# Kernel optimization log

Hardware: AMD Instinct MI355X
Metric: run time of the kernel (lower is better)

## Reference

```python
import jax, jax.numpy as jnp
import numpy as np

HEADS = 8
DIM_HEAD = 80
BATCH_SIZE = 2  # cfg batch (module init kwarg)


def setup_inputs() -> dict:
    key = jax.random.key(0)
    ks = jax.random.split(key, 6)
    F, S, D = 16, 1024, 640  # frames*batch, latent HW, query_dim
    hidden_states = jax.random.normal(ks[0], (F, S, D), jnp.float32)
    Wq = jax.random.normal(ks[1], (D, D), jnp.float32) * 0.02
    Wk = jax.random.normal(ks[2], (D, D), jnp.float32) * 0.02
    Wv = jax.random.normal(ks[3], (D, D), jnp.float32) * 0.02
    Wo = jax.random.normal(ks[4], (D, D), jnp.float32) * 0.02
    bo = jax.random.normal(ks[5], (D,), jnp.float32) * 0.02
    return {"hidden_states": hidden_states, "Wq": Wq, "Wk": Wk, "Wv": Wv, "Wo": Wo, "bo": bo}


def reference(hidden_states, Wq, Wk, Wv, Wo, bo):
    F, S, D = hidden_states.shape
    h, d = HEADS, DIM_HEAD
    scale = d ** -0.5

    q = hidden_states @ Wq  # [F, S, D]
    k = hidden_states @ Wk
    v = hidden_states @ Wv

    # cross-frame trick: replace every frame's K/V with the FIRST frame of its batch group
    vl = 1 if F < BATCH_SIZE else F // BATCH_SIZE  # video_length
    g = F // vl  # batch groups
    k = jnp.broadcast_to(k.reshape(g, vl, S, D)[:, :1], (g, vl, S, D)).reshape(F, S, D)
    v = jnp.broadcast_to(v.reshape(g, vl, S, D)[:, :1], (g, vl, S, D)).reshape(F, S, D)

    def to_heads(t):  # [F, S, h*d] -> [F*h, S, d]
        return t.reshape(F, S, h, d).transpose(0, 2, 1, 3).reshape(F * h, S, d)

    qh, kh, vh = to_heads(q), to_heads(k), to_heads(v)

    scores = jnp.einsum('bid,bjd->bij', qh, kh) * scale  # [F*h, S, S]
    probs = jax.nn.softmax(scores, axis=-1)
    out = jnp.einsum('bij,bjd->bid', probs, vh)  # [F*h, S, d]

    out = out.reshape(F, h, S, d).transpose(0, 2, 1, 3).reshape(F, S, h * d)
    return out @ Wo + bo
```

## Files before the change

kernel.cpp:

```cpp
#include <hip/hip_runtime.h>
#include <hip/hip_bf16.h>

typedef unsigned short u16;
typedef unsigned int u32;
typedef __attribute__((ext_vector_type(8))) short bf16x8;
typedef __attribute__((ext_vector_type(4))) float f32x4;

#define D640 640

__device__ __forceinline__ float b2f(u16 u) {
  union { u32 i; float f; } x; x.i = ((u32)u) << 16; return x.f;
}
__device__ __forceinline__ u16 f2b(float f) {
  union { __hip_bfloat16 h; u16 u; } c; c.h = __float2bfloat16(f); return c.u;
}
__device__ __forceinline__ u32 pack2(float a, float b) {
  union { __hip_bfloat162 h; u32 u; } c;
  c.h.x = __float2bfloat16(a); c.h.y = __float2bfloat16(b); return c.u;
}
__device__ __forceinline__ bf16x8 pack8(f32x4 lo, f32x4 hi) {
  bf16x8 r;
  r[0] = (short)f2b(lo[0]); r[1] = (short)f2b(lo[1]);
  r[2] = (short)f2b(lo[2]); r[3] = (short)f2b(lo[3]);
  r[4] = (short)f2b(hi[0]); r[5] = (short)f2b(hi[1]);
  r[6] = (short)f2b(hi[2]); r[7] = (short)f2b(hi[3]);
  return r;
}

__global__ void detect_dtype(const u16* __restrict__ hs, u32* __restrict__ flag) {
  __shared__ u32 cnt;
  if (threadIdx.x == 0) cnt = 0;
  __syncthreads();
  int plaus = 0;
#pragma unroll
  for (int i = 0; i < 16; ++i) {
    u16 u = hs[(threadIdx.x * 16 + i) * 2];
    u32 e = (u >> 7) & 0xFF;
    if ((e >= 0x70 && e <= 0x8F) || (u & 0x7FFF) == 0) plaus++;
  }
  atomicAdd(&cnt, (u32)plaus);
  __syncthreads();
  if (threadIdx.x == 0) *flag = (cnt < 2048) ? 1u : 0u;
}

__global__ __launch_bounds__(256) void transpose_w(
    const void* __restrict__ w0, const void* __restrict__ w1,
    const void* __restrict__ w2, const void* __restrict__ w3,
    u16* __restrict__ out, const u32* __restrict__ flag)
{
  __shared__ u16 t[32][33];
  const bool isF32 = (*flag != 0);
  const void* src = blockIdx.z == 0 ? w0 : blockIdx.z == 1 ? w1 : blockIdx.z == 2 ? w2 : w3;
  u16* dst = out + (size_t)blockIdx.z * 409600;
  int tx = threadIdx.x, ty = threadIdx.y;
  int x = blockIdx.x * 32 + tx;
  int y = blockIdx.y * 32 + ty;
  if (isF32) {
    const float* s = (const float*)src;
#pragma unroll
    for (int j = 0; j < 32; j += 8) t[ty + j][tx] = f2b(s[(y + j) * D640 + x]);
  } else {
    const u16* s = (const u16*)src;
#pragma unroll
    for (int j = 0; j < 32; j += 8) t[ty + j][tx] = s[(y + j) * D640 + x];
  }
  __syncthreads();
  int x2 = blockIdx.y * 32 + tx;
  int y2 = blockIdx.x * 32 + ty;
#pragma unroll
  for (int j = 0; j < 32; j += 8) dst[(y2 + j) * D640 + x2] = t[tx][ty + j];
}

__device__ __forceinline__ void gemm_body(
    const void* __restrict__ Av, const u16* __restrict__ BT, void* __restrict__ Cv,
    float scale, bool isF32, int aRow0, int cMode, int bx, int by)
{
  __shared__ __align__(16) u16 Asub[128 * 32];
  __shared__ __align__(16) u16 Bsub[128 * 32];
  const bool aF32 = isF32;
  const int tid = threadIdx.x;
  const int lane = tid & 63, w = tid >> 6;
  const int wr = w >> 1, wc = w & 1;
  const int l15 = lane & 15, g = lane >> 4;
  const int rowBase = bx * 128;
  const int colBase = by * 128;

  const int r0 = tid >> 2, r1 = r0 + 64, gc = tid & 3;
  const int ls0 = r0 * 4 + (gc ^ ((r0 >> 1) & 3));
  const int ls1 = r1 * 4 + (gc ^ ((r1 >> 1) & 3));
  const size_t aIdx0 = (size_t)(aRow0 + rowBase + r0) * D640 + gc * 8;
  const size_t aIdx1 = (size_t)(aRow0 + rowBase + r1) * D640 + gc * 8;
  const u16* Bg0 = BT + (colBase + r0) * D640 + gc * 8;
  const u16* Bg1 = BT + (colBase + r1) * D640 + gc * 8;

  int aoff[4], boff[4];
#pragma unroll
  for (int f = 0; f < 4; ++f) {
    int R = wr * 64 + f * 16 + l15;
    aoff[f] = (R * 4 + (g ^ ((R >> 1) & 3))) * 8;
    int Cc = wc * 64 + f * 16 + l15;
    boff[f] = (Cc * 4 + (g ^ ((Cc >> 1) & 3))) * 8;
  }

  f32x4 acc[4][4];
#pragma unroll
  for (int i = 0; i < 4; ++i)
#pragma unroll
    for (int j = 0; j < 4; ++j) acc[i][j] = (f32x4){0.f, 0.f, 0.f, 0.f};

  bf16x8 ra0, ra1, rb0, rb1;
  if (aF32) {
    const float* Af = (const float*)Av;
    ra0 = pack8(*(const f32x4*)(Af + aIdx0), *(const f32x4*)(Af + aIdx0 + 4));
    ra1 = pack8(*(const f32x4*)(Af + aIdx1), *(const f32x4*)(Af + aIdx1 + 4));
  } else {
    const u16* Ab = (const u16*)Av;
    ra0 = *(const bf16x8*)(Ab + aIdx0);
    ra1 = *(const bf16x8*)(Ab + aIdx1);
  }
  rb0 = *(const bf16x8*)Bg0;
  rb1 = *(const bf16x8*)Bg1;

  for (int kt = 0; kt < 20; ++kt) {
    __syncthreads();
    *(bf16x8*)&Asub[ls0 * 8] = ra0;
    *(bf16x8*)&Asub[ls1 * 8] = ra1;
    *(bf16x8*)&Bsub[ls0 * 8] = rb0;
    *(bf16x8*)&Bsub[ls1 * 8] = rb1;
    __syncthreads();
    if (kt < 19) {
      const int k1 = (kt + 1) * 32;
      if (aF32) {
        const float* Af = (const float*)Av;
        ra0 = pack8(*(const f32x4*)(Af + aIdx0 + k1), *(const f32x4*)(Af + aIdx0 + k1 + 4));
        ra1 = pack8(*(const f32x4*)(Af + aIdx1 + k1), *(const f32x4*)(Af + aIdx1 + k1 + 4));
      } else {
        const u16* Ab = (const u16*)Av;
        ra0 = *(const bf16x8*)(Ab + aIdx0 + k1);
        ra1 = *(const bf16x8*)(Ab + aIdx1 + k1);
      }
      rb0 = *(const bf16x8*)(Bg0 + k1);
      rb1 = *(const bf16x8*)(Bg1 + k1);
    }
    bf16x8 a[4], b[4];
#pragma unroll
    for (int f = 0; f < 4; ++f) a[f] = *(const bf16x8*)&Asub[aoff[f]];
#pragma unroll
    for (int f = 0; f < 4; ++f) b[f] = *(const bf16x8*)&Bsub[boff[f]];
    __builtin_amdgcn_s_setprio(1);
#pragma unroll
    for (int i = 0; i < 4; ++i)
#pragma unroll
      for (int j = 0; j < 4; ++j)
        acc[i][j] = __builtin_amdgcn_mfma_f32_16x16x32_bf16(a[i], b[j], acc[i][j], 0, 0, 0);
    __builtin_amdgcn_s_setprio(0);
  }

#pragma unroll
  for (int j = 0; j < 4; ++j) {
    int col = colBase + wc * 64 + j * 16 + l15;
#pragma unroll
    for (int i = 0; i < 4; ++i) {
      int row = rowBase + wr * 64 + i * 16 + g * 4;
#pragma unroll
      for (int r = 0; r < 4; ++r) {
        float v = acc[i][j][r] * scale;
        if (cMode == 2) {
          int rw = row + r;
          int rl = rw & 63;
          int slot = (rl & 32) | ((rl & 12) << 1) | (((rl >> 4) & 1) << 2) | (rl & 3);
          ((u16*)Cv)[(size_t)col * 1024 + (rw & ~63) + slot] = f2b(v);
        } else {
          ((u16*)Cv)[(size_t)(row + r) * D640 + col] = f2b(v);
        }
      }
    }
  }
}

__global__ __launch_bounds__(256) void gemm_kv(
    const void* __restrict__ hs, const u16* __restrict__ WTk, const u16* __restrict__ WTv,
    u16* __restrict__ Kb, u16* __restrict__ Vb, const u32* __restrict__ flag)
{
  const int z = blockIdx.z;
  const bool isK = (z < 2);
  const int grp = z & 1;
  const u16* bt = isK ? WTk : WTv;
  void* cv = isK ? (void*)(Kb + (size_t)grp * 1024 * 640)
                 : (void*)(Vb + (size_t)grp * 655360);
  gemm_body(hs, bt, cv, 1.f, (*flag != 0), grp * 8192, isK ? 0 : 2,
            blockIdx.x, blockIdx.y);
}

__global__ __launch_bounds__(256) void gemm2(
    const void* __restrict__ Av, const u16* __restrict__ BT, void* __restrict__ Cv,
    float scale, const void* __restrict__ bias, const u32* __restrict__ flag,
    int aF32mode, int cF32mode)
{
  __shared__ __align__(16) u16 Asub[128 * 32];
  __shared__ __align__(16) u16 Bsub[160 * 32];
  const bool isF32 = (*flag != 0);
  const bool aF32 = aF32mode && isF32;
  const bool cF32 = cF32mode && isF32;
  const int tid = threadIdx.x;
  const int lane = tid & 63, w = tid >> 6;
  const int wr = w >> 1, wc = w & 1;
  const int l15 = lane & 15, g = lane >> 4;
  const int rowBase = blockIdx.x * 128;
  const int colBase = blockIdx.y * 160;

  const int ar0 = tid >> 2, ar1 = ar0 + 64, gc = tid & 3;
  const int als0 = ar0 * 4 + (gc ^ ((ar0 >> 1) & 3));
  const int als1 = ar1 * 4 + (gc ^ ((ar1 >> 1) & 3));
  const size_t aIdx0 = (size_t)(rowBase + ar0) * D640 + gc * 8;
  const size_t aIdx1 = (size_t)(rowBase + ar1) * D640 + gc * 8;
  const bool hasB3 = (tid < 128);
  const int br0 = ar0, br1 = ar1, br2 = hasB3 ? (128 + (tid >> 2)) : 0;
  const int bls0 = als0, bls1 = als1;
  const int bls2 = br2 * 4 + (gc ^ ((br2 >> 1) & 3));
  const u16* Bg0 = BT + (colBase + br0) * D640 + gc * 8;
  const u16* Bg1 = BT + (colBase + br1) * D640 + gc * 8;
  const u16* Bg2 = BT + (colBase + br2) * D640 + gc * 8;

  int aoff[4], boff[5];
#pragma unroll
  for (int f = 0; f < 4; ++f) {
    int R = wr * 64 + f * 16 + l15;
    aoff[f] = (R * 4 + (g ^ ((R >> 1) & 3))) * 8;
  }
#pragma unroll
  for (int j = 0; j < 5; ++j) {
    int Cc = wc * 80 + j * 16 + l15;
    boff[j] = (Cc * 4 + (g ^ ((Cc >> 1) & 3))) * 8;
  }

  f32x4 acc[4][5];
#pragma unroll
  for (int i = 0; i < 4; ++i)
#pragma unroll
    for (int j = 0; j < 5; ++j) acc[i][j] = (f32x4){0.f, 0.f, 0.f, 0.f};

  bf16x8 ra0, ra1, rb0, rb1, rb2;
  if (aF32) {
    const float* Af = (const float*)Av;
    ra0 = pack8(*(const f32x4*)(Af + aIdx0), *(const f32x4*)(Af + aIdx0 + 4));
    ra1 = pack8(*(const f32x4*)(Af + aIdx1), *(const f32x4*)(Af + aIdx1 + 4));
  } else {
    const u16* Ab = (const u16*)Av;
    ra0 = *(const bf16x8*)(Ab + aIdx0);
    ra1 = *(const bf16x8*)(Ab + aIdx1);
  }
  rb0 = *(const bf16x8*)Bg0;
  rb1 = *(const bf16x8*)Bg1;
  rb2 = hasB3 ? *(const bf16x8*)Bg2 : (bf16x8){0,0,0,0,0,0,0,0};

  for (int kt = 0; kt < 20; ++kt) {
    __syncthreads();
    *(bf16x8*)&Asub[als0 * 8] = ra0;
    *(bf16x8*)&Asub[als1 * 8] = ra1;
    *(bf16x8*)&Bsub[bls0 * 8] = rb0;
    *(bf16x8*)&Bsub[bls1 * 8] = rb1;
    if (hasB3) *(bf16x8*)&Bsub[bls2 * 8] = rb2;
    __syncthreads();
    if (kt < 19) {
      const int k1 = (kt + 1) * 32;
      if (aF32) {
        const float* Af = (const float*)Av;
        ra0 = pack8(*(const f32x4*)(Af + aIdx0 + k1), *(const f32x4*)(Af + aIdx0 + k1 + 4));
        ra1 = pack8(*(const f32x4*)(Af + aIdx1 + k1), *(const f32x4*)(Af + aIdx1 + k1 + 4));
      } else {
        const u16* Ab = (const u16*)Av;
        ra0 = *(const bf16x8*)(Ab + aIdx0 + k1);
        ra1 = *(const bf16x8*)(Ab + aIdx1 + k1);
      }
      rb0 = *(const bf16x8*)(Bg0 + k1);
      rb1 = *(const bf16x8*)(Bg1 + k1);
      if (hasB3) rb2 = *(const bf16x8*)(Bg2 + k1);
    }
    bf16x8 a[4], b[5];
#pragma unroll
    for (int f = 0; f < 4; ++f) a[f] = *(const bf16x8*)&Asub[aoff[f]];
#pragma unroll
    for (int j = 0; j < 5; ++j) b[j] = *(const bf16x8*)&Bsub[boff[j]];
    __builtin_amdgcn_s_setprio(1);
#pragma unroll
    for (int i = 0; i < 4; ++i)
#pragma unroll
      for (int j = 0; j < 5; ++j)
        acc[i][j] = __builtin_amdgcn_mfma_f32_16x16x32_bf16(a[i], b[j], acc[i][j], 0, 0, 0);
    __builtin_amdgcn_s_setprio(0);
  }

#pragma unroll
  for (int j = 0; j < 5; ++j) {
    int col = colBase + wc * 80 + j * 16 + l15;
    float bb = 0.f;
    if (bias) bb = cF32 ? ((const float*)bias)[col] : b2f(((const u16*)bias)[col]);
#pragma unroll
    for (int i = 0; i < 4; ++i) {
      int row = rowBase + wr * 64 + i * 16 + g * 4;
#pragma unroll
      for (int r = 0; r < 4; ++r) {
        float v = acc[i][j][r] * scale + bb;
        if (cF32) ((float*)Cv)[(size_t)(row + r) * D640 + col] = v;
        else      ((u16*)Cv)[(size_t)(row + r) * D640 + col] = f2b(v);
      }
    }
  }
}

__global__ __launch_bounds__(256, 3) void attn_kernel(
    const u16* __restrict__ Q, const u16* __restrict__ K2,
    const u16* __restrict__ VT, u16* __restrict__ AO)
{
  __shared__ __align__(16) u16 Klds[64 * 104];
  __shared__ __align__(16) u16 Vlds[80 * 72];

  const int tid = threadIdx.x, lane = tid & 63, w = tid >> 6;
  const int l15 = lane & 15, g = lane >> 4;
  const int qc = blockIdx.x, bh = blockIdx.y;
  const int f = bh >> 3, h = bh & 7;
  const int grp = f >> 3;

  const u16* Qp = Q + (size_t)(f * 1024 + qc * 128 + w * 32) * D640 + h * 80;
  const u16* Kp = K2 + (size_t)(grp * 1024) * D640 + h * 80;
  const u16* Vp = VT + (size_t)(grp * 8 + h) * 80 * 1024;

  if (tid < 128) {
    const bf16x8 z8 = {0, 0, 0, 0, 0, 0, 0, 0};
    *(bf16x8*)&Klds[(tid >> 1) * 104 + 80 + (tid & 1) * 8] = z8;
  }

  bf16x8 qreg[2][3];
#pragma unroll
  for (int qb = 0; qb < 2; ++qb)
#pragma unroll
    for (int dc = 0; dc < 3; ++dc) {
      int dd = dc * 32 + g * 8;
      if (dd < 80) qreg[qb][dc] = *(const bf16x8*)(Qp + (l15 + 16 * qb) * D640 + dd);
      else         qreg[qb][dc] = (bf16x8){0, 0, 0, 0, 0, 0, 0, 0};
    }

  f32x4 acc[2][5];
#pragma unroll
  for (int qb = 0; qb < 2; ++qb)
#pragma unroll
    for (int db = 0; db < 5; ++db) acc[qb][db] = (f32x4){0.f, 0.f, 0.f, 0.f};
  float mreg[2] = {-1e30f, -1e30f};
  float lrow[2] = {0.f, 0.f};

  const u16* gsrc[5];
  u16* ldst[5];
  int step[5];
#pragma unroll
  for (int i = 0; i < 5; ++i) {
    int c = tid + i * 256;
    if (c < 640) {
      int row = c / 10, cc = c - row * 10;
      gsrc[i] = Kp + row * D640 + cc * 8;
      ldst[i] = &Klds[row * 104 + cc * 8];
      step[i] = 64 * D640;
    } else {
      int c2 = c - 640, d = c2 >> 3, cc = c2 & 7;
      gsrc[i] = Vp + d * 1024 + cc * 8;
      ldst[i] = &Vlds[d * 72 + cc * 8];
      step[i] = 64;
    }
  }

  bf16x8 pre[5];
#pragma unroll
  for (int i = 0; i < 5; ++i) pre[i] = *(const bf16x8*)gsrc[i];

  for (int it = 0; it < 16; ++it) {
    __syncthreads();
#pragma unroll
    for (int i = 0; i < 5; ++i) *(bf16x8*)ldst[i] = pre[i];
    __syncthreads();
    if (it < 15) {
#pragma unroll
      for (int i = 0; i < 5; ++i) pre[i] = *(const bf16x8*)(gsrc[i] + (it + 1) * step[i]);
    }

    f32x4 st[4][2];
#pragma unroll
    for (int kb = 0; kb < 4; ++kb)
#pragma unroll
      for (int qb = 0; qb < 2; ++qb) st[kb][qb] = (f32x4){0.f, 0.f, 0.f, 0.f};
    __builtin_amdgcn_s_setprio(1);
#pragma unroll
    for (int dc = 0; dc < 3; ++dc)
#pragma unroll
      for (int kb = 0; kb < 4; ++kb) {
        bf16x8 ka = *(const bf16x8*)&Klds[(kb * 16 + l15) * 104 + dc * 32 + g * 8];
        st[kb][0] = __builtin_amdgcn_mfma_f32_16x16x32_bf16(ka, qreg[0][dc], st[kb][0], 0, 0, 0);
        st[kb][1] = __builtin_amdgcn_mfma_f32_16x16x32_bf16(ka, qreg[1][dc], st[kb][1], 0, 0, 0);
      }
    __builtin_amdgcn_s_setprio(0);

    float mt[2];
#pragma unroll
    for (int qb = 0; qb < 2; ++qb) {
      float m01 = fmaxf(fmaxf(st[0][qb][0], st[0][qb][1]), fmaxf(st[0][qb][2], st[0][qb][3]));
      float m23 = fmaxf(fmaxf(st[1][qb][0], st[1][qb][1]), fmaxf(st[1][qb][2], st[1][qb][3]));
      float m45 = fmaxf(fmaxf(st[2][qb][0], st[2][qb][1]), fmaxf(st[2][qb][2], st[2][qb][3]));
      float m67 = fmaxf(fmaxf(st[3][qb][0], st[3][qb][1]), fmaxf(st[3][qb][2], st[3][qb][3]));
      float m = fmaxf(fmaxf(m01, m23), fmaxf(m45, m67));
      m = fmaxf(m, __shfl_xor(m, 16, 64));
      m = fmaxf(m, __shfl_xor(m, 32, 64));
      mt[qb] = m;
    }

    if (__any((mt[0] > mreg[0] + 8.f) || (mt[1] > mreg[1] + 8.f))) {
#pragma unroll
      for (int qb = 0; qb < 2; ++qb) {
        float mn = fmaxf(mreg[qb], mt[qb]);
        float scl = exp2f(mreg[qb] - mn);
        mreg[qb] = mn;
        lrow[qb] *= scl;
        float s_[4];
#pragma unroll
        for (int r = 0; r < 4; ++r)
          s_[r] = __shfl(scl, (lane & 48) | (g * 4 + r), 64);
#pragma unroll
        for (int db = 0; db < 5; ++db)
#pragma unroll
          for (int r = 0; r < 4; ++r) acc[qb][db][r] *= s_[r];
      }
    }

    bf16x8 pa[2][2];
#pragma unroll
    for (int qb = 0; qb < 2; ++qb) {
      float sum = 0.f;
      u32 wlo[4], whi[4];
#pragma unroll
      for (int kb = 0; kb < 4; ++kb) {
        float p0 = exp2f(st[kb][qb][0] - mreg[qb]);
        float p1 = exp2f(st[kb][qb][1] - mreg[qb]);
        float p2 = exp2f(st[kb][qb][2] - mreg[qb]);
        float p3 = exp2f(st[kb][qb][3] - mreg[qb]);
        sum += (p0 + p1) + (p2 + p3);
        wlo[kb] = pack2(p0, p1);
        whi[kb] = pack2(p2, p3);
      }
      sum += __shfl_xor(sum, 16, 64);
      sum += __shfl_xor(sum, 32, 64);
      lrow[qb] += sum;
#pragma unroll
      for (int kc = 0; kc < 2; ++kc) {
        union { u32 u[4]; bf16x8 v; } cvt;
        cvt.u[0] = wlo[2 * kc];
        cvt.u[1] = whi[2 * kc];
        cvt.u[2] = wlo[2 * kc + 1];
        cvt.u[3] = whi[2 * kc + 1];
        pa[qb][kc] = cvt.v;
      }
    }

    __builtin_amdgcn_s_setprio(1);
#pragma unroll
    for (int kc = 0; kc < 2; ++kc) {
#pragma unroll
      for (int db = 0; db < 5; ++db) {
        bf16x8 bv = *(const bf16x8*)&Vlds[(db * 16 + l15) * 72 + kc * 32 + g * 8];
        acc[0][db] = __builtin_amdgcn_mfma_f32_16x16x32_bf16(pa[0][kc], bv, acc[0][db], 0, 0, 0);
        acc[1][db] = __builtin_amdgcn_mfma_f32_16x16x32_bf16(pa[1][kc], bv, acc[1][db], 0, 0, 0);
      }
    }
    __builtin_amdgcn_s_setprio(0);
  }

  u16* Op = AO + (size_t)(f * 1024 + qc * 128 + w * 32) * D640 + h * 80;
#pragma unroll
  for (int qb = 0; qb < 2; ++qb) {
    float i_[4];
#pragma unroll
    for (int r = 0; r < 4; ++r)
      i_[r] = 1.f / __shfl(lrow[qb], (lane & 48) | (g * 4 + r), 64);
#pragma unroll
    for (int db = 0; db < 5; ++db)
#pragma unroll
      for (int r = 0; r < 4; ++r)
        Op[(qb * 16 + g * 4 + r) * D640 + db * 16 + l15] = f2b(acc[qb][db][r] * i_[r]);
  }
}

extern "C" void kernel_launch(void* const* d_in, const int* in_sizes, int n_in,
                              void* d_out, int out_size, void* d_ws, size_t ws_size,
                              hipStream_t stream) {
  (void)in_sizes; (void)n_in; (void)out_size; (void)ws_size;
  const void* hs = d_in[0];
  const void* wq = d_in[1];
  const void* wk = d_in[2];
  const void* wv = d_in[3];
  const void* wo = d_in[4];
  const void* bo = d_in[5];
  u16* ws = (u16*)d_ws;

  u16* WT  = ws;
  u16* Qb  = ws + 1638400;
  u16* Kb  = Qb + 10485760;
  u16* Vb  = Kb + 1310720;
  u16* AOb = Vb + 1310720;
  u32* flag = (u32*)(AOb + 10485760);

  const float QSCALE = 0.11180339887498949f * 1.44269504088896340f;

  detect_dtype<<<1, 256, 0, stream>>>((const u16*)hs, flag);

  transpose_w<<<dim3(20, 20, 4), dim3(32, 8), 0, stream>>>(wq, wk, wv, wo, WT, flag);

  gemm2<<<dim3(128, 4), 256, 0, stream>>>(hs, WT, Qb, QSCALE, nullptr, flag, 1, 0);
  gemm_kv<<<dim3(8, 5, 4), 256, 0, stream>>>(hs, WT + 409600, WT + 819200, Kb, Vb, flag);

  attn_kernel<<<dim3(8, 128), 256, 0, stream>>>(Qb, Kb, Vb, AOb);

  gemm2<<<dim3(128, 4), 256, 0, stream>>>(AOb, WT + 1228800, d_out, 1.f, bo, flag, 0, 1);
}
```

Baseline: 169.6 us.

## Use direct global-to-LDS loads in output GEMM and defer softmax row reductions

Adds a new output-projection GEMM with 128x128 tiles that loads A and B tiles straight from global memory into XOR-swizzled shared memory through global_load_lds, replacing the register-staged gemm2 for that step. In attention, the cross-lane row max reduction now runs only inside the rare rescale branch, and the row-sum reduction is deferred to the epilogue. The running max starts at zero instead of a very negative value. This cuts shuffle work per key tile and register staging in the GEMM, but the attention rescale is now driven by each lane's partial max and loads are not double-buffered.

New measurement: 164.3 us. 3.1% less time.

```diff
diff --git a/kernel.cpp b/kernel.cpp
--- a/kernel.cpp
+++ b/kernel.cpp
@@ -25,6 +25,10 @@
   r[4] = (short)f2b(hi[0]); r[5] = (short)f2b(hi[1]);
   r[6] = (short)f2b(hi[2]); r[7] = (short)f2b(hi[3]);
   return r;
+}
+__device__ __forceinline__ void gld_lds16(const u16* g, u16* l) {
+  __builtin_amdgcn_global_load_lds((const __attribute__((address_space(1))) u32*)g,
+                                   (__attribute__((address_space(3))) u32*)l, 16, 0, 0);
 }
 
 __global__ void detect_dtype(const u16* __restrict__ hs, u32* __restrict__ flag) {
@@ -186,7 +190,7 @@
   const bool isK = (z < 2);
   const int grp = z & 1;
   const u16* bt = isK ? WTk : WTv;
-  void* cv = isK ? (void*)(Kb + (size_t)grp * 1024 * 640)
+  void* cv = isK ? (void*)(Kb + (size_t)grp * 655360)
                  : (void*)(Vb + (size_t)grp * 655360);
   gemm_body(hs, bt, cv, 1.f, (*flag != 0), grp * 8192, isK ? 0 : 2,
             blockIdx.x, blockIdx.y);
@@ -309,6 +313,86 @@
   }
 }
 
+__global__ __launch_bounds__(256) void gemm3(
+    const u16* __restrict__ A, const u16* __restrict__ BT, void* __restrict__ Cv,
+    float scale, const void* __restrict__ bias, const u32* __restrict__ flag,
+    int aRow0, int cMode)
+{
+  __shared__ __align__(16) u16 Asub[128 * 32];
+  __shared__ __align__(16) u16 Bsub[128 * 32];
+  const bool isF32 = (*flag != 0);
+  const bool cF32 = (cMode == 1) && isF32;
+  const int tid = threadIdx.x;
+  const int lane = tid & 63, w = tid >> 6;
+  const int wr = w >> 1, wc = w & 1;
+  const int l15 = lane & 15, g = lane >> 4;
+  const int rowBase = blockIdx.x * 128;
+  const int colBase = blockIdx.y * 128;
+
+  const int c0 = w * 128 + lane, c1 = c0 + 64;
+  const u16* Ag0 = A + (size_t)(aRow0 + rowBase + (c0 >> 2)) * D640 + ((c0 & 3) ^ ((c0 >> 3) & 3)) * 8;
+  const u16* Ag1 = A + (size_t)(aRow0 + rowBase + (c1 >> 2)) * D640 + ((c1 & 3) ^ ((c1 >> 3) & 3)) * 8;
+  const u16* Bg0 = BT + (size_t)(colBase + (c0 >> 2)) * D640 + ((c0 & 3) ^ ((c0 >> 3) & 3)) * 8;
+  const u16* Bg1 = BT + (size_t)(colBase + (c1 >> 2)) * D640 + ((c1 & 3) ^ ((c1 >> 3) & 3)) * 8;
+  u16* lA0 = &Asub[w * 1024];
+  u16* lA1 = &Asub[w * 1024 + 512];
+  u16* lB0 = &Bsub[w * 1024];
+  u16* lB1 = &Bsub[w * 1024 + 512];
+
+  int aoff[4], boff[4];
+#pragma unroll
+  for (int f = 0; f < 4; ++f) {
+    int R = wr * 64 + f * 16 + l15;
+    aoff[f] = (R * 4 + (g ^ ((R >> 1) & 3))) * 8;
+    int Cc = wc * 64 + f * 16 + l15;
+    boff[f] = (Cc * 4 + (g ^ ((Cc >> 1) & 3))) * 8;
+  }
+
+  f32x4 acc[4][4];
+#pragma unroll
+  for (int i = 0; i < 4; ++i)
+#pragma unroll
+    for (int j = 0; j < 4; ++j) acc[i][j] = (f32x4){0.f, 0.f, 0.f, 0.f};
+
+  for (int kt = 0; kt < 20; ++kt) {
+    __syncthreads();
+    gld_lds16(Ag0 + kt * 32, lA0);
+    gld_lds16(Ag1 + kt * 32, lA1);
+    gld_lds16(Bg0 + kt * 32, lB0);
+    gld_lds16(Bg1 + kt * 32, lB1);
+    __syncthreads();
+    bf16x8 a[4], b[4];
+#pragma unroll
+    for (int f = 0; f < 4; ++f) a[f] = *(const bf16x8*)&Asub[aoff[f]];
+#pragma unroll
+    for (int f = 0; f < 4; ++f) b[f] = *(const bf16x8*)&Bsub[boff[f]];
+    __builtin_amdgcn_s_setprio(1);
+#pragma unroll
+    for (int i = 0; i < 4; ++i)
+#pragma unroll
+      for (int j = 0; j < 4; ++j)
+        acc[i][j] = __builtin_amdgcn_mfma_f32_16x16x32_bf16(a[i], b[j], acc[i][j], 0, 0, 0);
+    __builtin_amdgcn_s_setprio(0);
+  }
+
+#pragma unroll
+  for (int j = 0; j < 4; ++j) {
+    int col = colBase + wc * 64 + j * 16 + l15;
+    float bb = 0.f;
+    if (bias) bb = cF32 ? ((const float*)bias)[col] : b2f(((const u16*)bias)[col]);
+#pragma unroll
+    for (int i = 0; i < 4; ++i) {
+      int row = rowBase + wr * 64 + i * 16 + g * 4;
+#pragma unroll
+      for (int r = 0; r < 4; ++r) {
+        float v = acc[i][j][r] * scale + bb;
+        if (cF32) ((float*)Cv)[(size_t)(row + r) * D640 + col] = v;
+        else      ((u16*)Cv)[(size_t)(row + r) * D640 + col] = f2b(v);
+      }
+    }
+  }
+}
+
 __global__ __launch_bounds__(256, 3) void attn_kernel(
     const u16* __restrict__ Q, const u16* __restrict__ K2,
     const u16* __restrict__ VT, u16* __restrict__ AO)
@@ -346,7 +430,7 @@
   for (int qb = 0; qb < 2; ++qb)
 #pragma unroll
     for (int db = 0; db < 5; ++db) acc[qb][db] = (f32x4){0.f, 0.f, 0.f, 0.f};
-  float mreg[2] = {-1e30f, -1e30f};
+  float mreg[2] = {0.f, 0.f};
   float lrow[2] = {0.f, 0.f};
 
   const u16* gsrc[5];
@@ -405,16 +489,16 @@
       float m23 = fmaxf(fmaxf(st[1][qb][0], st[1][qb][1]), fmaxf(st[1][qb][2], st[1][qb][3]));
       float m45 = fmaxf(fmaxf(st[2][qb][0], st[2][qb][1]), fmaxf(st[2][qb][2], st[2][qb][3]));
       float m67 = fmaxf(fmaxf(st[3][qb][0], st[3][qb][1]), fmaxf(st[3][qb][2], st[3][qb][3]));
-      float m = fmaxf(fmaxf(m01, m23), fmaxf(m45, m67));
-      m = fmaxf(m, __shfl_xor(m, 16, 64));
-      m = fmaxf(m, __shfl_xor(m, 32, 64));
-      mt[qb] = m;
+      mt[qb] = fmaxf(fmaxf(m01, m23), fmaxf(m45, m67));
     }
 
     if (__any((mt[0] > mreg[0] + 8.f) || (mt[1] > mreg[1] + 8.f))) {
 #pragma unroll
       for (int qb = 0; qb < 2; ++qb) {
-        float mn = fmaxf(mreg[qb], mt[qb]);
+        float m = mt[qb];
+        m = fmaxf(m, __shfl_xor(m, 16, 64));
+        m = fmaxf(m, __shfl_xor(m, 32, 64));
+        float mn = fmaxf(mreg[qb], m);
         float scl = exp2f(mreg[qb] - mn);
         mreg[qb] = mn;
         lrow[qb] *= scl;
@@ -444,8 +528,6 @@
         wlo[kb] = pack2(p0, p1);
         whi[kb] = pack2(p2, p3);
       }
-      sum += __shfl_xor(sum, 16, 64);
-      sum += __shfl_xor(sum, 32, 64);
       lrow[qb] += sum;
 #pragma unroll
       for (int kc = 0; kc < 2; ++kc) {
@@ -474,10 +556,13 @@
   u16* Op = AO + (size_t)(f * 1024 + qc * 128 + w * 32) * D640 + h * 80;
 #pragma unroll
   for (int qb = 0; qb < 2; ++qb) {
+    float lr = lrow[qb];
+    lr += __shfl_xor(lr, 16, 64);
+    lr += __shfl_xor(lr, 32, 64);
     float i_[4];
 #pragma unroll
     for (int r = 0; r < 4; ++r)
-      i_[r] = 1.f / __shfl(lrow[qb], (lane & 48) | (g * 4 + r), 64);
+      i_[r] = 1.f / __shfl(lr, (lane & 48) | (g * 4 + r), 64);
 #pragma unroll
     for (int db = 0; db < 5; ++db)
 #pragma unroll
@@ -508,7 +593,6 @@
   const float QSCALE = 0.11180339887498949f * 1.44269504088896340f;
 
   detect_dtype<<<1, 256, 0, stream>>>((const u16*)hs, flag);
-
   transpose_w<<<dim3(20, 20, 4), dim3(32, 8), 0, stream>>>(wq, wk, wv, wo, WT, flag);
 
   gemm2<<<dim3(128, 4), 256, 0, stream>>>(hs, WT, Qb, QSCALE, nullptr, flag, 1, 0);
@@ -516,5 +600,5 @@
 
   attn_kernel<<<dim3(8, 128), 256, 0, stream>>>(Qb, Kb, Vb, AOb);
 
-  gemm2<<<dim3(128, 4), 256, 0, stream>>>(AOb, WT + 1228800, d_out, 1.f, bo, flag, 0, 1);
-}
+  gemm3<<<dim3(128, 5), 256, 0, stream>>>(AOb, WT + 1228800, d_out, 1.f, bo, flag, 0, 1);
+}
```
